# Kernel optimization log

Measured on AMD Instinct MI355X. Metric: run time of the kernel, lower is better.

## Reference

```python
import jax, jax.numpy as jnp
import numpy as np

B = 64        # graphs
N = 2048      # nodes per graph (equal-sized graphs -> regular top-k)
D = 128       # in_channels
RATIO = 0.5
E = 4_194_304 # edges (avg degree 32)
K = int(np.ceil(RATIO * N))  # nodes kept per graph = 1024


def setup_inputs() -> dict:
    key = jax.random.key(0)
    k1, k2, k3 = jax.random.split(key, 3)
    x = jax.random.normal(k1, (B * N, D), dtype=jnp.float32)
    edge_index = jax.random.randint(k2, (2, E), 0, B * N, dtype=jnp.int32)
    batch = jnp.repeat(jnp.arange(B, dtype=jnp.int32), N)  # node i -> graph i//N
    w = jax.random.normal(k3, (D,), dtype=jnp.float32)     # TopKPooling scoring weight
    return {"x": x, "edge_index": edge_index, "batch": batch, "w": w}


def reference(x, edge_index, batch, w):
    # PyG TopKPooling: score = nonlinearity((x . w) / ||w||), default nonlinearity = tanh
    score = jnp.tanh((x @ w) / jnp.linalg.norm(w))               # [B*N]
    # per-graph top-k (graphs are equal-sized -> reshape + lax.top_k)
    top_vals, top_idx = jax.lax.top_k(score.reshape(B, N), K)    # [B, K] each
    offsets = (jnp.arange(B, dtype=top_idx.dtype) * N)[:, None]
    perm = (top_idx + offsets).reshape(-1)                       # [B*K] global node ids
    score_sel = top_vals.reshape(-1)                             # [B*K]
    # gate selected node features by their score
    x_out = x[perm] * score_sel[:, None]                         # [B*K, D]
    # relabel nodes: old id -> new compacted id, -1 if dropped
    new_idx = jnp.full((B * N,), -1, dtype=jnp.int32).at[perm].set(
        jnp.arange(B * K, dtype=jnp.int32))
    nr = new_idx[edge_index[0]]
    nc = new_idx[edge_index[1]]
    edge_mask = (nr >= 0) & (nc >= 0)                            # [E] kept edges
    edge_index_out = jnp.where(edge_mask, jnp.stack([nr, nc]), 0)  # fixed-shape, masked
    batch_out = jnp.repeat(jnp.arange(B, dtype=jnp.int32), K)
    return x_out, edge_index_out, batch_out, perm, score_sel, edge_mask
```

## Files before the change

kernel.cpp:

```cpp
#include <hip/hip_runtime.h>
#include <math.h>

#define BG 64
#define NN 2048
#define DD 128
#define KK 1024
#define EE 4194304

#define OFF_EI   8388608
#define OFF_BAT  16777216
#define OFF_PERM 16842752
#define OFF_SCR  16908288
#define OFF_MSK  16973824

#define EDGE_BLOCKS   1024
#define GATHER_BLOCKS 2048

typedef unsigned long long u64;
typedef float f4v __attribute__((ext_vector_type(4)));
typedef int   i4v __attribute__((ext_vector_type(4)));

__device__ __forceinline__ void nt_store4(float a, float b, float c, float d, float* p) {
    f4v v = {a, b, c, d};
    __builtin_nontemporal_store(v, (f4v*)p);
}

__global__ __launch_bounds__(256) void score_kernel(
    const float2* __restrict__ x2, const float2* __restrict__ w2,
    float* __restrict__ scores)
{
    int node = (blockIdx.x * 256 + threadIdx.x) >> 6;
    int lane = threadIdx.x & 63;
    float2 xv = x2[(size_t)node * 64 + lane];
    float2 wv = w2[lane];
    float dot = xv.x * wv.x + xv.y * wv.y;
    float ww  = wv.x * wv.x + wv.y * wv.y;
    #pragma unroll
    for (int off = 32; off >= 1; off >>= 1) {
        dot += __shfl_xor(dot, off);
        ww  += __shfl_xor(ww, off);
    }
    if (lane == 0) scores[node] = tanhf(dot / sqrtf(ww));
}

__device__ __forceinline__ unsigned ford(float f) {
    unsigned b = __float_as_uint(f);
    return (b & 0x80000000u) ? ~b : (b | 0x80000000u);
}
__device__ __forceinline__ float forddec(unsigned u) {
    unsigned b = (u & 0x80000000u) ? (u & 0x7FFFFFFFu) : ~u;
    return __uint_as_float(b);
}

__device__ __forceinline__ u64 regswap(u64 v, int elem_idx, int j, int k) {
    u64 p = __shfl_xor(v, j, 64);
    bool dir   = ((elem_idx & k) == 0);
    bool lower = ((elem_idx & j) == 0);
    return (dir == lower) ? (v > p ? v : p) : (v < p ? v : p);
}

__global__ __launch_bounds__(1024) void sort_kernel(
    const float* __restrict__ scores,
    int* __restrict__ perm_int, unsigned short* __restrict__ tab16,
    unsigned* __restrict__ maskbits,
    float* __restrict__ out_batch, float* __restrict__ out_perm,
    float* __restrict__ out_score)
{
    __shared__ u64 keys[NN];
    __shared__ unsigned mw[NN / 32];
    const int b = blockIdx.x;
    const int t = threadIdx.x;

    float s0 = scores[b * NN + t];
    float s1 = scores[b * NN + 1024 + t];
    u64 va = ((u64)ford(s0) << 32) | (unsigned)(NN - 1 - t);
    u64 vb = ((u64)ford(s1) << 32) | (unsigned)(NN - 1 - (1024 + t));

    #pragma unroll
    for (int k = 2; k <= 64; k <<= 1)
        #pragma unroll
        for (int j = k >> 1; j >= 1; j >>= 1) {
            va = regswap(va, t, j, k);
            vb = regswap(vb, 1024 + t, j, k);
        }

    keys[t] = va; keys[1024 + t] = vb;
    if (t < NN / 32) mw[t] = 0u;
    __syncthreads();

    for (int k = 128; k <= 2048; k <<= 1) {
        for (int j = k >> 1; j >= 64; j >>= 1) {
            int i = ((t & ~(j - 1)) << 1) | (t & (j - 1));
            int p = i | j;
            u64 A = keys[i], C = keys[p];
            bool sw = ((i & k) == 0) ? (A < C) : (A > C);
            if (sw) { keys[i] = C; keys[p] = A; }
            __syncthreads();
        }
        va = keys[t]; vb = keys[1024 + t];
        #pragma unroll
        for (int j = 32; j >= 1; j >>= 1) {
            va = regswap(va, t, j, k);
            vb = regswap(vb, 1024 + t, j, k);
        }
        if (k < 2048) {
            keys[t] = va; keys[1024 + t] = vb;
            __syncthreads();
        }
    }

    int idx  = NN - 1 - (int)(va & 0xFFFFFFFFu);
    float s  = forddec((unsigned)(va >> 32));
    int gid  = b * NN + idx;
    int row  = b * KK + t;
    perm_int[row]  = gid;
    tab16[gid]     = (unsigned short)row;
    out_perm[row]  = (float)gid;
    out_score[row] = s;
    out_batch[row] = (float)b;
    atomicOr(&mw[idx >> 5], 1u << (idx & 31));
    __syncthreads();
    if (t < NN / 32) maskbits[b * (NN / 32) + t] = mw[t];
}

__global__ __launch_bounds__(256) void tail_kernel(
    const int* __restrict__ e0, const int* __restrict__ e1,
    const unsigned* __restrict__ mb, const unsigned short* __restrict__ tab,
    const float4* __restrict__ x4, const int* __restrict__ perm_int,
    const float* __restrict__ out_score, float* __restrict__ out)
{
    __shared__ unsigned smask[BG * NN / 32];
    int bid = blockIdx.x;
    int t   = threadIdx.x;
    if (bid < EDGE_BLOCKS) {
        const uint4* mb4 = (const uint4*)mb;
        uint4* sm4 = (uint4*)smask;
        #pragma unroll
        for (int u = 0; u < 4; ++u)
            sm4[u * 256 + t] = mb4[u * 256 + t];
        __syncthreads();

        float* oe0 = out + OFF_EI;
        float* oe1 = out + OFF_EI + EE;
        float* om  = out + OFF_MSK;

        size_t eb = (size_t)bid * 1024 + t;
        i4v r[4], c[4];
        #pragma unroll
        for (int u = 0; u < 4; ++u) {
            r[u] = __builtin_nontemporal_load((const i4v*)e0 + eb + u * 256);
            c[u] = __builtin_nontemporal_load((const i4v*)e1 + eb + u * 256);
        }
        #pragma unroll
        for (int u = 0; u < 4; ++u) {
            size_t i = eb + u * 256;
            float er[4], ec[4], em[4];
            #pragma unroll
            for (int q = 0; q < 4; ++q) {
                int rq = r[u][q], cq = c[u][q];
                unsigned m = (smask[(unsigned)rq >> 5] >> (rq & 31)) &
                             (smask[(unsigned)cq >> 5] >> (cq & 31)) & 1u;
                float nr = 0.0f, nc = 0.0f;
                if (m) {
                    nr = (float)tab[rq];
                    nc = (float)tab[cq];
                }
                er[q] = nr; ec[q] = nc; em[q] = m ? 1.0f : 0.0f;
            }
            nt_store4(er[0], er[1], er[2], er[3], oe0 + 4 * i);
            nt_store4(ec[0], ec[1], ec[2], ec[3], oe1 + 4 * i);
            nt_store4(em[0], em[1], em[2], em[3], om  + 4 * i);
        }
    } else {
        int gb   = bid - EDGE_BLOCKS;
        int lane = t & 31;
        int rbase = gb * 32 + (t >> 5);
        int g[4]; float s[4];
        #pragma unroll
        for (int p = 0; p < 4; ++p) {
            int row = rbase + p * 8;
            g[p] = perm_int[row];
            s[p] = out_score[row];
        }
        float4 v[4];
        #pragma unroll
        for (int p = 0; p < 4; ++p)
            v[p] = x4[(size_t)g[p] * 32 + lane];
        #pragma unroll
        for (int p = 0; p < 4; ++p) {
            int row = rbase + p * 8;
            nt_store4(v[p].x * s[p], v[p].y * s[p], v[p].z * s[p], v[p].w * s[p],
                      out + ((size_t)row * 32 + lane) * 4);
        }
    }
}

extern "C" void kernel_launch(void* const* d_in, const int* in_sizes, int n_in,
                              void* d_out, int out_size, void* d_ws, size_t ws_size,
                              hipStream_t stream)
{
    const float* x  = (const float*)d_in[0];
    const int*   ei = (const int*)d_in[1];
    const float* w  = (const float*)d_in[3];
    float* out = (float*)d_out;

    float*          scores   = (float*)d_ws;
    int*            perm_i   = (int*)d_ws + BG * NN;
    unsigned short* tab16    = (unsigned short*)((char*)d_ws + (BG * NN + BG * KK) * 4);
    unsigned*       maskbits = (unsigned*)((char*)d_ws + (BG * NN + BG * KK) * 4 + BG * NN * 2);

    score_kernel<<<BG * NN / 4, 256, 0, stream>>>(
        (const float2*)x, (const float2*)w, scores);

    sort_kernel<<<BG, 1024, 0, stream>>>(
        scores, perm_i, tab16, maskbits,
        out + OFF_BAT, out + OFF_PERM, out + OFF_SCR);

    tail_kernel<<<EDGE_BLOCKS + GATHER_BLOCKS, 256, 0, stream>>>(
        ei, ei + EE, maskbits, tab16,
        (const float4*)x, perm_i, out + OFF_SCR, out);
}
```

Baseline: 66.23 us.

## Fuse score, sort and tail into one cooperative kernel with grid syncs

Merges the three kernels into one cooperative launch of 256 blocks of 1024 threads, separated by grid-wide syncs. This removes launch gaps between stages. While 64 blocks run the per-graph bitonic sort, the other blocks stream edge_index through a dummy XOR reduction to warm the cache for the later edge pass. The costs are grid.sync overhead, only 256 resident blocks doing the score and gather phases, and the edge loads no longer being nontemporal.

```diff
diff --git a/kernel.cpp b/kernel.cpp
--- a/kernel.cpp
+++ b/kernel.cpp
@@ -1,9 +1,11 @@
 #include <hip/hip_runtime.h>
+#include <hip/hip_cooperative_groups.h>
 #include <math.h>
+
+namespace cg = cooperative_groups;
 
 #define BG 64
 #define NN 2048
-#define DD 128
 #define KK 1024
 #define EE 4194304
 
@@ -13,8 +15,8 @@
 #define OFF_SCR  16908288
 #define OFF_MSK  16973824
 
-#define EDGE_BLOCKS   1024
-#define GATHER_BLOCKS 2048
+#define NBLK 256
+#define NTHR 1024
 
 typedef unsigned long long u64;
 typedef float f4v __attribute__((ext_vector_type(4)));
@@ -23,24 +25,6 @@
 __device__ __forceinline__ void nt_store4(float a, float b, float c, float d, float* p) {
     f4v v = {a, b, c, d};
     __builtin_nontemporal_store(v, (f4v*)p);
-}
-
-__global__ __launch_bounds__(256) void score_kernel(
-    const float2* __restrict__ x2, const float2* __restrict__ w2,
-    float* __restrict__ scores)
-{
-    int node = (blockIdx.x * 256 + threadIdx.x) >> 6;
-    int lane = threadIdx.x & 63;
-    float2 xv = x2[(size_t)node * 64 + lane];
-    float2 wv = w2[lane];
-    float dot = xv.x * wv.x + xv.y * wv.y;
-    float ww  = wv.x * wv.x + wv.y * wv.y;
-    #pragma unroll
-    for (int off = 32; off >= 1; off >>= 1) {
-        dot += __shfl_xor(dot, off);
-        ww  += __shfl_xor(ww, off);
-    }
-    if (lane == 0) scores[node] = tanhf(dot / sqrtf(ww));
 }
 
 __device__ __forceinline__ unsigned ford(float f) {
@@ -59,101 +43,129 @@
     return (dir == lower) ? (v > p ? v : p) : (v < p ? v : p);
 }
 
-__global__ __launch_bounds__(1024) void sort_kernel(
-    const float* __restrict__ scores,
-    int* __restrict__ perm_int, unsigned short* __restrict__ tab16,
-    unsigned* __restrict__ maskbits,
-    float* __restrict__ out_batch, float* __restrict__ out_perm,
-    float* __restrict__ out_score)
+__global__ __launch_bounds__(NTHR, 4) void fused_kernel(
+    const float* __restrict__ x, const int* __restrict__ ei,
+    const float* __restrict__ w, float* __restrict__ out,
+    float* __restrict__ scores, int* __restrict__ perm_int,
+    unsigned short* __restrict__ tab16, unsigned* __restrict__ maskbits)
 {
-    __shared__ u64 keys[NN];
-    __shared__ unsigned mw[NN / 32];
-    const int b = blockIdx.x;
-    const int t = threadIdx.x;
-
-    float s0 = scores[b * NN + t];
-    float s1 = scores[b * NN + 1024 + t];
-    u64 va = ((u64)ford(s0) << 32) | (unsigned)(NN - 1 - t);
-    u64 vb = ((u64)ford(s1) << 32) | (unsigned)(NN - 1 - (1024 + t));
-
-    #pragma unroll
-    for (int k = 2; k <= 64; k <<= 1)
-        #pragma unroll
-        for (int j = k >> 1; j >= 1; j >>= 1) {
-            va = regswap(va, t, j, k);
-            vb = regswap(vb, 1024 + t, j, k);
-        }
-
-    keys[t] = va; keys[1024 + t] = vb;
-    if (t < NN / 32) mw[t] = 0u;
-    __syncthreads();
-
-    for (int k = 128; k <= 2048; k <<= 1) {
-        for (int j = k >> 1; j >= 64; j >>= 1) {
-            int i = ((t & ~(j - 1)) << 1) | (t & (j - 1));
-            int p = i | j;
-            u64 A = keys[i], C = keys[p];
-            bool sw = ((i & k) == 0) ? (A < C) : (A > C);
-            if (sw) { keys[i] = C; keys[p] = A; }
-            __syncthreads();
-        }
-        va = keys[t]; vb = keys[1024 + t];
-        #pragma unroll
-        for (int j = 32; j >= 1; j >>= 1) {
-            va = regswap(va, t, j, k);
-            vb = regswap(vb, 1024 + t, j, k);
-        }
-        if (k < 2048) {
-            keys[t] = va; keys[1024 + t] = vb;
-            __syncthreads();
-        }
-    }
-
-    int idx  = NN - 1 - (int)(va & 0xFFFFFFFFu);
-    float s  = forddec((unsigned)(va >> 32));
-    int gid  = b * NN + idx;
-    int row  = b * KK + t;
-    perm_int[row]  = gid;
-    tab16[gid]     = (unsigned short)row;
-    out_perm[row]  = (float)gid;
-    out_score[row] = s;
-    out_batch[row] = (float)b;
-    atomicOr(&mw[idx >> 5], 1u << (idx & 31));
-    __syncthreads();
-    if (t < NN / 32) maskbits[b * (NN / 32) + t] = mw[t];
-}
-
-__global__ __launch_bounds__(256) void tail_kernel(
-    const int* __restrict__ e0, const int* __restrict__ e1,
-    const unsigned* __restrict__ mb, const unsigned short* __restrict__ tab,
-    const float4* __restrict__ x4, const int* __restrict__ perm_int,
-    const float* __restrict__ out_score, float* __restrict__ out)
-{
-    __shared__ unsigned smask[BG * NN / 32];
-    int bid = blockIdx.x;
-    int t   = threadIdx.x;
-    if (bid < EDGE_BLOCKS) {
-        const uint4* mb4 = (const uint4*)mb;
-        uint4* sm4 = (uint4*)smask;
-        #pragma unroll
-        for (int u = 0; u < 4; ++u)
-            sm4[u * 256 + t] = mb4[u * 256 + t];
+    __shared__ u64 shbuf[NN + 32];
+    cg::grid_group grid = cg::this_grid();
+    const int bid = blockIdx.x;
+    const int t   = threadIdx.x;
+
+    {
+        const float2* x2 = (const float2*)x;
+        const float2* w2 = (const float2*)w;
+        int lane = t & 63;
+        int wavg = bid * 16 + (t >> 6);
+        float2 wv = w2[lane];
+        float ww = wv.x * wv.x + wv.y * wv.y;
+        #pragma unroll
+        for (int off = 32; off >= 1; off >>= 1) ww += __shfl_xor(ww, off);
+        int nbase = wavg * 32;
+        for (int n = 0; n < 32; ++n) {
+            int node = nbase + n;
+            float2 xv = x2[(size_t)node * 64 + lane];
+            float dot = xv.x * wv.x + xv.y * wv.y;
+            #pragma unroll
+            for (int off = 32; off >= 1; off >>= 1) dot += __shfl_xor(dot, off);
+            if (lane == 0) scores[node] = tanhf(dot / sqrtf(ww));
+        }
+    }
+    __threadfence();
+    grid.sync();
+
+    if (bid < BG) {
+        u64* keys = shbuf;
+        unsigned* mw = (unsigned*)(shbuf + NN);
+        const int b = bid;
+        float s0 = scores[b * NN + t];
+        float s1 = scores[b * NN + 1024 + t];
+        u64 va = ((u64)ford(s0) << 32) | (unsigned)(NN - 1 - t);
+        u64 vb = ((u64)ford(s1) << 32) | (unsigned)(NN - 1 - (1024 + t));
+
+        #pragma unroll
+        for (int k = 2; k <= 64; k <<= 1)
+            #pragma unroll
+            for (int j = k >> 1; j >= 1; j >>= 1) {
+                va = regswap(va, t, j, k);
+                vb = regswap(vb, 1024 + t, j, k);
+            }
+
+        keys[t] = va; keys[1024 + t] = vb;
+        if (t < NN / 32) mw[t] = 0u;
         __syncthreads();
 
+        for (int k = 128; k <= 2048; k <<= 1) {
+            for (int j = k >> 1; j >= 64; j >>= 1) {
+                int i = ((t & ~(j - 1)) << 1) | (t & (j - 1));
+                int p = i | j;
+                u64 A = keys[i], C = keys[p];
+                bool sw = ((i & k) == 0) ? (A < C) : (A > C);
+                if (sw) { keys[i] = C; keys[p] = A; }
+                __syncthreads();
+            }
+            va = keys[t]; vb = keys[1024 + t];
+            #pragma unroll
+            for (int j = 32; j >= 1; j >>= 1) {
+                va = regswap(va, t, j, k);
+                vb = regswap(vb, 1024 + t, j, k);
+            }
+            if (k < 2048) {
+                keys[t] = va; keys[1024 + t] = vb;
+                __syncthreads();
+            }
+        }
+
+        int idx  = NN - 1 - (int)(va & 0xFFFFFFFFu);
+        float s  = forddec((unsigned)(va >> 32));
+        int gid  = b * NN + idx;
+        int row  = b * KK + t;
+        perm_int[row]       = gid;
+        tab16[gid]          = (unsigned short)row;
+        out[OFF_PERM + row] = (float)gid;
+        out[OFF_SCR + row]  = s;
+        out[OFF_BAT + row]  = (float)b;
+        atomicOr(&mw[idx >> 5], 1u << (idx & 31));
+        __syncthreads();
+        if (t < NN / 32) maskbits[b * (NN / 32) + t] = mw[t];
+    } else {
+        const i4v* e4 = (const i4v*)ei;
+        const int total4 = 2 * EE / 4;
+        int tid = (bid - BG) * NTHR + t;
+        int acc = 0;
+        for (size_t i = tid; i < (size_t)total4; i += (size_t)(NBLK - BG) * NTHR) {
+            i4v v = e4[i];
+            acc ^= v[0] ^ v[1] ^ v[2] ^ v[3];
+        }
+        asm volatile("" :: "v"(acc));
+    }
+    __threadfence();
+    grid.sync();
+
+    unsigned* smask = (unsigned*)shbuf;
+    {
+        const uint4* mb4 = (const uint4*)maskbits;
+        ((uint4*)smask)[t] = mb4[t];
+        __syncthreads();
+    }
+    {
+        const int* e0 = ei;
+        const int* e1 = ei + EE;
         float* oe0 = out + OFF_EI;
         float* oe1 = out + OFF_EI + EE;
         float* om  = out + OFF_MSK;
-
-        size_t eb = (size_t)bid * 1024 + t;
+        size_t eb = (size_t)bid * 4096 + t;
         i4v r[4], c[4];
         #pragma unroll
         for (int u = 0; u < 4; ++u) {
-            r[u] = __builtin_nontemporal_load((const i4v*)e0 + eb + u * 256);
-            c[u] = __builtin_nontemporal_load((const i4v*)e1 + eb + u * 256);
+            r[u] = ((const i4v*)e0)[eb + u * 1024];
+            c[u] = ((const i4v*)e1)[eb + u * 1024];
         }
         #pragma unroll
         for (int u = 0; u < 4; ++u) {
-            size_t i = eb + u * 256;
+            size_t i = eb + u * 1024;
             float er[4], ec[4], em[4];
             #pragma unroll
             for (int q = 0; q < 4; ++q) {
@@ -162,8 +174,8 @@
                              (smask[(unsigned)cq >> 5] >> (cq & 31)) & 1u;
                 float nr = 0.0f, nc = 0.0f;
                 if (m) {
-                    nr = (float)tab[rq];
-                    nc = (float)tab[cq];
+                    nr = (float)tab16[rq];
+                    nc = (float)tab16[cq];
                 }
                 er[q] = nr; ec[q] = nc; em[q] = m ? 1.0f : 0.0f;
             }
@@ -171,26 +183,30 @@
             nt_store4(ec[0], ec[1], ec[2], ec[3], oe1 + 4 * i);
             nt_store4(em[0], em[1], em[2], em[3], om  + 4 * i);
         }
-    } else {
-        int gb   = bid - EDGE_BLOCKS;
+    }
+    {
+        const float4* x4 = (const float4*)x;
         int lane = t & 31;
-        int rbase = gb * 32 + (t >> 5);
-        int g[4]; float s[4];
-        #pragma unroll
-        for (int p = 0; p < 4; ++p) {
-            int row = rbase + p * 8;
-            g[p] = perm_int[row];
-            s[p] = out_score[row];
-        }
-        float4 v[4];
-        #pragma unroll
-        for (int p = 0; p < 4; ++p)
-            v[p] = x4[(size_t)g[p] * 32 + lane];
-        #pragma unroll
-        for (int p = 0; p < 4; ++p) {
-            int row = rbase + p * 8;
-            nt_store4(v[p].x * s[p], v[p].y * s[p], v[p].z * s[p], v[p].w * s[p],
-                      out + ((size_t)row * 32 + lane) * 4);
+        int grp  = t >> 5;
+        #pragma unroll
+        for (int pass = 0; pass < 2; ++pass) {
+            int g[4]; float s[4];
+            #pragma unroll
+            for (int p = 0; p < 4; ++p) {
+                int row = bid * 256 + grp + (pass * 4 + p) * 32;
+                g[p] = perm_int[row];
+                s[p] = out[OFF_SCR + row];
+            }
+            float4 v[4];
+            #pragma unroll
+            for (int p = 0; p < 4; ++p)
+                v[p] = x4[(size_t)g[p] * 32 + lane];
+            #pragma unroll
+            for (int p = 0; p < 4; ++p) {
+                int row = bid * 256 + grp + (pass * 4 + p) * 32;
+                nt_store4(v[p].x * s[p], v[p].y * s[p], v[p].z * s[p], v[p].w * s[p],
+                          out + ((size_t)row * 32 + lane) * 4);
+            }
         }
     }
 }
@@ -209,14 +225,8 @@
     unsigned short* tab16    = (unsigned short*)((char*)d_ws + (BG * NN + BG * KK) * 4);
     unsigned*       maskbits = (unsigned*)((char*)d_ws + (BG * NN + BG * KK) * 4 + BG * NN * 2);
 
-    score_kernel<<<BG * NN / 4, 256, 0, stream>>>(
-        (const float2*)x, (const float2*)w, scores);
-
-    sort_kernel<<<BG, 1024, 0, stream>>>(
-        scores, perm_i, tab16, maskbits,
-        out + OFF_BAT, out + OFF_PERM, out + OFF_SCR);
-
-    tail_kernel<<<EDGE_BLOCKS + GATHER_BLOCKS, 256, 0, stream>>>(
-        ei, ei + EE, maskbits, tab16,
-        (const float4*)x, perm_i, out + OFF_SCR, out);
-}
+    void* args[] = { (void*)&x, (void*)&ei, (void*)&w, (void*)&out,
+                     (void*)&scores, (void*)&perm_i, (void*)&tab16, (void*)&maskbits };
+    hipLaunchCooperativeKernel((const void*)fused_kernel,
+                               dim3(NBLK), dim3(NTHR), args, 0, stream);
+}
```

Measured after the change: 258.7 us. +290.5%, slower.
